# Performance work log

Hardware: AMD Instinct MI355X
Metric: run time of the kernel (lower is better)

## Reference

```python
import jax, jax.numpy as jnp
import numpy as np

EMB = 1024
HEADS = 16
HEAD_DIM = EMB // HEADS
SEQ = 2048
BATCH = 2
EPS = 1e-5


def gelu_tanh(x):
    # 0.5*x*(1+tanh(sqrt(2/pi)*(x+0.044715*x^3)))
    c = jnp.sqrt(jnp.asarray(2.0 / jnp.pi, x.dtype))
    return 0.5 * x * (1.0 + jnp.tanh(c * (x + 0.044715 * x * x * x)))


def layernorm(x, scale, shift):
    mean = jnp.mean(x, axis=-1, keepdims=True)
    # torch var(unbiased=True) -> ddof=1
    var = jnp.var(x, axis=-1, keepdims=True, ddof=1)
    return scale * (x - mean) / jnp.sqrt(var + EPS) + shift


def setup_inputs() -> dict:
    key = jax.random.key(0)
    ks = jax.random.split(key, 12)
    s = 0.02
    d = {
        "x": jax.random.normal(ks[0], (BATCH, SEQ, EMB), jnp.float32),
        "Wq": jax.random.normal(ks[1], (EMB, EMB), jnp.float32) * s,
        "bq": jnp.zeros((EMB,), jnp.float32),
        "Wk": jax.random.normal(ks[2], (EMB, EMB), jnp.float32) * s,
        "bk": jnp.zeros((EMB,), jnp.float32),
        "Wv": jax.random.normal(ks[3], (EMB, EMB), jnp.float32) * s,
        "bv": jnp.zeros((EMB,), jnp.float32),
        "Wo": jax.random.normal(ks[4], (EMB, EMB), jnp.float32) * s,
        "bo": jnp.zeros((EMB,), jnp.float32),
        "W1": jax.random.normal(ks[5], (EMB, 4 * EMB), jnp.float32) * s,
        "b1": jnp.zeros((4 * EMB,), jnp.float32),
        "W2": jax.random.normal(ks[6], (4 * EMB, EMB), jnp.float32) * s,
        "b2": jnp.zeros((EMB,), jnp.float32),
        "ln1_scale": jnp.ones((EMB,), jnp.float32),
        "ln1_shift": jnp.zeros((EMB,), jnp.float32),
        "ln2_scale": jnp.ones((EMB,), jnp.float32),
        "ln2_shift": jnp.zeros((EMB,), jnp.float32),
    }
    return d


def reference(x, Wq, bq, Wk, bk, Wv, bv, Wo, bo, W1, b1, W2, b2,
              ln1_scale, ln1_shift, ln2_scale, ln2_shift):
    b, n, _ = x.shape

    # --- attention sub-block (pre-norm) ---
    h = layernorm(x, ln1_scale, ln1_shift)
    q = (h @ Wq + bq).reshape(b, n, HEADS, HEAD_DIM).transpose(0, 2, 1, 3)
    k = (h @ Wk + bk).reshape(b, n, HEADS, HEAD_DIM).transpose(0, 2, 1, 3)
    v = (h @ Wv + bv).reshape(b, n, HEADS, HEAD_DIM).transpose(0, 2, 1, 3)

    # explicit O(n^2) scores, as in the source
    scores = jnp.einsum("bhqd,bhkd->bhqk", q, k)
    causal = jnp.triu(jnp.ones((n, n), bool), k=1)  # True above diagonal -> masked
    scores = jnp.where(causal, -jnp.inf, scores)
    weights = jax.nn.softmax(scores / jnp.sqrt(jnp.asarray(HEAD_DIM, x.dtype)), axis=-1)
    ctx = jnp.einsum("bhqk,bhkd->bhqd", weights, v)
    ctx = ctx.transpose(0, 2, 1, 3).reshape(b, n, EMB)
    x = x + (ctx @ Wo + bo)  # dropout is identity (rate 0 / eval)

    # --- FFN sub-block (pre-norm) ---
    h = layernorm(x, ln2_scale, ln2_shift)
    h = gelu_tanh(h @ W1 + b1)
    x = x + (h @ W2 + b2)
    return x
```

## Files before the change

kernel.cpp:

```cpp
#include <hip/hip_runtime.h>
#include <hip/hip_bf16.h>

#define EMB 1024
#define SEQ 2048
#define BATCH 2
#define HEADS 16
#define HDIM 64
#define ROWS (BATCH*SEQ)

typedef __hip_bfloat16 bf16;
typedef __bf16 bf16x8 __attribute__((ext_vector_type(8)));
typedef float f32x4 __attribute__((ext_vector_type(4)));

#define AS1 __attribute__((address_space(1)))
#define AS3 __attribute__((address_space(3)))

__device__ __forceinline__ void load_lds16(const void* g, void* l) {
    __builtin_amdgcn_global_load_lds((const AS1 void*)g, (AS3 void*)l, 16, 0, 0);
}

__device__ __forceinline__ float gelu_f(float x) {
    float y = 1.5957691216057308f * (x + 0.044715f * x * x * x);
    return x / (1.0f + __expf(-y));
}

__global__ void transpose_cast_kernel(const float* __restrict__ in, bf16* __restrict__ out,
                                      int R, int C) {
    __shared__ bf16 tile[32][33];
    int tx = threadIdx.x, ty = threadIdx.y;
    int c0 = blockIdx.x * 32, r0 = blockIdx.y * 32;
    for (int i = ty; i < 32; i += 8)
        tile[i][tx] = (bf16)in[(size_t)(r0 + i) * C + c0 + tx];
    __syncthreads();
    for (int i = ty; i < 32; i += 8)
        out[(size_t)(c0 + i) * R + r0 + tx] = tile[tx][i];
}

__global__ void transpose_cast4_kernel(const float* __restrict__ w0, const float* __restrict__ w1,
                                       const float* __restrict__ w2, const float* __restrict__ w3,
                                       bf16* __restrict__ o0, bf16* __restrict__ o1,
                                       bf16* __restrict__ o2, bf16* __restrict__ o3) {
    __shared__ bf16 tile[32][33];
    int z = blockIdx.z;
    const float* in = (z == 0) ? w0 : (z == 1) ? w1 : (z == 2) ? w2 : w3;
    bf16* out = (z == 0) ? o0 : (z == 1) ? o1 : (z == 2) ? o2 : o3;
    int tx = threadIdx.x, ty = threadIdx.y;
    int c0 = blockIdx.x * 32, r0 = blockIdx.y * 32;
    for (int i = ty; i < 32; i += 8)
        tile[i][tx] = (bf16)in[(size_t)(r0 + i) * 1024 + c0 + tx];
    __syncthreads();
    for (int i = ty; i < 32; i += 8)
        out[(size_t)(c0 + i) * 1024 + r0 + tx] = tile[tx][i];
}

__global__ void transpose_v_kernel(const bf16* __restrict__ v, bf16* __restrict__ vt) {
    __shared__ bf16 tile[32][33];
    int tx = threadIdx.x, ty = threadIdx.y;
    int bh = blockIdx.z;
    const bf16* in = v + (size_t)(bh >> 4) * SEQ * EMB + (bh & 15) * HDIM;
    bf16* out = vt + (size_t)bh * HDIM * SEQ;
    int s0 = blockIdx.x * 32, d0 = blockIdx.y * 32;
    for (int i = ty; i < 32; i += 8)
        tile[i][tx] = in[(size_t)(s0 + i) * EMB + d0 + tx];
    __syncthreads();
    for (int i = ty; i < 32; i += 8)
        out[(size_t)(d0 + i) * SEQ + s0 + tx] = tile[tx][i];
}

__global__ __launch_bounds__(256) void layernorm_kernel(const float* __restrict__ x,
                                                        bf16* __restrict__ out,
                                                        const float* __restrict__ scale,
                                                        const float* __restrict__ shift) {
    int row = blockIdx.x;
    int t = threadIdx.x;
    const float* xr = x + (size_t)row * EMB;
    float v[4];
    float s = 0.f, s2 = 0.f;
#pragma unroll
    for (int i = 0; i < 4; i++) {
        v[i] = xr[t + 256 * i];
        s += v[i];
        s2 += v[i] * v[i];
    }
#pragma unroll
    for (int off = 32; off > 0; off >>= 1) {
        s += __shfl_down(s, off);
        s2 += __shfl_down(s2, off);
    }
    __shared__ float sh[8];
    __shared__ float stats[2];
    int lane = t & 63, wid = t >> 6;
    if (lane == 0) { sh[wid] = s; sh[wid + 4] = s2; }
    __syncthreads();
    if (t == 0) {
        float ts = sh[0] + sh[1] + sh[2] + sh[3];
        float ts2 = sh[4] + sh[5] + sh[6] + sh[7];
        float mean = ts / (float)EMB;
        float var = (ts2 - (float)EMB * mean * mean) / (float)(EMB - 1);
        stats[0] = mean;
        stats[1] = rsqrtf(var + 1e-5f);
    }
    __syncthreads();
    float mean = stats[0], inv = stats[1];
#pragma unroll
    for (int i = 0; i < 4; i++) {
        int c = t + 256 * i;
        float y = (v[i] - mean) * inv * scale[c] + shift[c];
        out[(size_t)row * EMB + c] = (bf16)y;
    }
}

__device__ __forceinline__ void swz64(int id, int& bx, int& by) {
    int xcd = id & 7, m = id >> 3;
    by = xcd + 8 * (m & 3) + 32 * (m >> 6);
    bx = (m >> 2) & 15;
}

__device__ __forceinline__ void stage_half(const bf16* g, bf16* lds, int tid, size_t rowK64) {
    load_lds16(g, lds + tid * 8);
    load_lds16(g + rowK64, lds + 4096 + tid * 8);
}

template <int ACT, int QKV>
__global__ __launch_bounds__(512, 2) void gemm256_kernel(
    const bf16* __restrict__ A, const bf16* __restrict__ BT,
    bf16* __restrict__ C0, bf16* __restrict__ C1, bf16* __restrict__ C2,
    const float* __restrict__ bias0, const float* __restrict__ bias1,
    const float* __restrict__ bias2, int N, int K) {
    __shared__ __align__(16) bf16 lA[4][128 * 64];
    __shared__ __align__(16) bf16 lB[4][128 * 64];
    const int tid = threadIdx.x;
    const int wave = tid >> 6, lane = tid & 63;
    const int an = lane & 15, aq = lane >> 4;
    const int wr = wave >> 2, wc = wave & 3;

    int id = blockIdx.x;
    int xcd = id & 7, m = id >> 3;
    int by = xcd * 2 + (m & 1);
    int bx = m >> 1;
    int m0 = by * 256, n0 = bx * 256;

    const int srow = tid >> 3;
    const int csw = ((tid & 7) ^ (srow & 7)) * 8;
    const bf16* Ag = A + (size_t)(m0 + srow) * K + csw;
    const bf16* Bg = BT + (size_t)(n0 + srow) * K + csw;
    const size_t rowK64 = (size_t)64 * K;
    const size_t rowK128 = (size_t)128 * K;

    stage_half(Bg, lB[0], tid, rowK64);
    stage_half(Bg + rowK128, lB[1], tid, rowK64);
    stage_half(Ag, lA[0], tid, rowK64);
    stage_half(Ag + rowK128, lA[1], tid, rowK64);
    stage_half(Bg + 64, lB[2], tid, rowK64);
    stage_half(Bg + rowK128 + 64, lB[3], tid, rowK64);
    asm volatile("s_waitcnt vmcnt(4)" ::: "memory");
    __builtin_amdgcn_s_barrier();

    f32x4 acc[8][4] = {};
    const int NT = K >> 6;
    const int lrB = (wc & 1) * 64;

    for (int t = 0; t < NT; ++t) {
        const bf16* As = lA[(2 * t + wr) & 3];
        const bf16* Bs = lB[(2 * t + (wc >> 1)) & 3];
        bf16x8 bfv[4][2];
#pragma unroll
        for (int p = 0; p < 4; ++p) {
            bf16x8 af[2][2];
            if (p == 0) {
#pragma unroll
                for (int j = 0; j < 4; ++j)
#pragma unroll
                    for (int kk = 0; kk < 2; ++kk) {
                        int r = lrB + 16 * j + an;
                        bfv[j][kk] = *(const bf16x8*)(Bs + r * 64 + ((kk * 4 + aq) ^ (r & 7)) * 8);
                    }
            }
#pragma unroll
            for (int ii = 0; ii < 2; ++ii)
#pragma unroll
                for (int kk = 0; kk < 2; ++kk) {
                    int r = 16 * (2 * p + ii) + an;
                    af[ii][kk] = *(const bf16x8*)(As + r * 64 + ((kk * 4 + aq) ^ (r & 7)) * 8);
                }
            if (p == 0) {
                if (t + 1 < NT)
                    stage_half(Ag + (size_t)(t + 1) * 64, lA[(2 * t + 2) & 3], tid, rowK64);
            } else if (p == 1) {
                if (t + 1 < NT)
                    stage_half(Ag + rowK128 + (size_t)(t + 1) * 64, lA[(2 * t + 3) & 3], tid, rowK64);
            } else if (p == 2) {
                if (t + 2 < NT)
                    stage_half(Bg + (size_t)(t + 2) * 64, lB[(2 * t + 4) & 3], tid, rowK64);
            } else {
                if (t + 2 < NT) {
                    stage_half(Bg + rowK128 + (size_t)(t + 2) * 64, lB[(2 * t + 5) & 3], tid, rowK64);
                    asm volatile("s_waitcnt vmcnt(4)" ::: "memory");
                } else {
                    asm volatile("s_waitcnt vmcnt(0)" ::: "memory");
                }
            }
            __builtin_amdgcn_s_barrier();
            asm volatile("s_waitcnt lgkmcnt(0)" ::: "memory");
            __builtin_amdgcn_s_setprio(1);
#pragma unroll
            for (int ii = 0; ii < 2; ++ii)
#pragma unroll
                for (int j = 0; j < 4; ++j)
#pragma unroll
                    for (int kk = 0; kk < 2; ++kk)
                        acc[2 * p + ii][j] = __builtin_amdgcn_mfma_f32_16x16x32_bf16(
                            af[ii][kk], bfv[j][kk], acc[2 * p + ii][j], 0, 0, 0);
            __builtin_amdgcn_s_setprio(0);
            __builtin_amdgcn_s_barrier();
        }
    }

#pragma unroll
    for (int j = 0; j < 4; ++j) {
        int col = n0 + wc * 64 + 16 * j + an;
        if (QKV == 0) {
            float bv = bias0[col];
#pragma unroll
            for (int i = 0; i < 8; ++i) {
#pragma unroll
                for (int r = 0; r < 4; ++r) {
                    int row = m0 + wr * 128 + 16 * i + aq * 4 + r;
                    float v = acc[i][j][r] + bv;
                    if (ACT == 1) v = gelu_f(v);
                    C0[(size_t)row * N + col] = (bf16)v;
                }
            }
        } else {
            int region = col >> 10, c = col & 1023;
            const float* bp = (region == 0) ? bias0 : (region == 1) ? bias1 : bias2;
            bf16* outp = (region == 0) ? C0 : (region == 1) ? C1 : C2;
            float scl = (region == 0) ? 0.125f : 1.0f;
            float bv = bp[c];
#pragma unroll
            for (int i = 0; i < 8; ++i) {
#pragma unroll
                for (int r = 0; r < 4; ++r) {
                    int row = m0 + wr * 128 + 16 * i + aq * 4 + r;
                    float v = (acc[i][j][r] + bv) * scl;
                    outp[(size_t)row * EMB + c] = (bf16)v;
                }
            }
        }
    }
}

template <int RES, int OUTF>
__global__ __launch_bounds__(256) void gemm64_kernel(const bf16* __restrict__ A,
                                                     const bf16* __restrict__ BT,
                                                     void* __restrict__ Cout,
                                                     const float* __restrict__ bias,
                                                     const float* __restrict__ res,
                                                     int M, int N, int K) {
    __shared__ __align__(16) bf16 lA[2][2][64 * 32];
    __shared__ __align__(16) bf16 lB[2][2][64 * 32];
    int tid = threadIdx.x;
    int wave = tid >> 6, lane = tid & 63;
    int bx, by;
    swz64(blockIdx.x, bx, by);
    int m0 = by * 64, n0 = bx * 64;
    int wm = (wave >> 1) * 32, wn = (wave & 1) * 32;
    f32x4 acc[2][2] = {};

    int srow = wave * 16 + (lane >> 2);
    int skc = (lane & 3) * 8;
    const bf16* Ag = A + (size_t)(m0 + srow) * K + skc;
    const bf16* Bg = BT + (size_t)(n0 + srow) * K + skc;
    size_t woff = (size_t)(wave * 16) * 32;

    const int an = lane & 15;
    const int ak = (lane >> 4) * 8;

    load_lds16(Ag, &lA[0][0][woff]);
    load_lds16(Ag + 32, &lA[0][1][woff]);
    load_lds16(Bg, &lB[0][0][woff]);
    load_lds16(Bg + 32, &lB[0][1][woff]);

    int nsteps = K >> 6;
    for (int t = 0; t < nsteps; t++) {
        int buf = t & 1;
        asm volatile("s_waitcnt vmcnt(0)" ::: "memory");
        __syncthreads();
        if (t + 1 < nsteps) {
            int k0 = (t + 1) * 64;
            load_lds16(Ag + k0, &lA[buf ^ 1][0][woff]);
            load_lds16(Ag + k0 + 32, &lA[buf ^ 1][1][woff]);
            load_lds16(Bg + k0, &lB[buf ^ 1][0][woff]);
            load_lds16(Bg + k0 + 32, &lB[buf ^ 1][1][woff]);
        }
#pragma unroll
        for (int h = 0; h < 2; h++) {
            bf16x8 af[2], bfv[2];
#pragma unroll
            for (int i = 0; i < 2; i++)
                af[i] = *(const bf16x8*)(&lA[buf][h][(wm + 16 * i + an) * 32 + ak]);
#pragma unroll
            for (int j = 0; j < 2; j++)
                bfv[j] = *(const bf16x8*)(&lB[buf][h][(wn + 16 * j + an) * 32 + ak]);
#pragma unroll
            for (int i = 0; i < 2; i++)
#pragma unroll
                for (int j = 0; j < 2; j++)
                    acc[i][j] = __builtin_amdgcn_mfma_f32_16x16x32_bf16(af[i], bfv[j], acc[i][j], 0, 0, 0);
        }
    }
#pragma unroll
    for (int j = 0; j < 2; j++) {
        int col = n0 + wn + 16 * j + an;
        float bv = bias[col];
#pragma unroll
        for (int i = 0; i < 2; i++) {
#pragma unroll
            for (int r = 0; r < 4; r++) {
                int row = m0 + wm + 16 * i + (lane >> 4) * 4 + r;
                float vx = acc[i][j][r] + bv;
                size_t idx = (size_t)row * N + col;
                if (RES == 2) vx += res[idx];
                if (OUTF == 0) ((bf16*)Cout)[idx] = (bf16)vx;
                else ((float*)Cout)[idx] = vx;
            }
        }
    }
}

__global__ __launch_bounds__(256) void attn_kernel(const bf16* __restrict__ q,
                                                   const bf16* __restrict__ k,
                                                   const bf16* __restrict__ vt,
                                                   bf16* __restrict__ ctx) {
    __shared__ __align__(16) bf16 ksm[2][2048];
    __shared__ __align__(16) bf16 vsm[2][2048];
    __shared__ __align__(16) bf16 pbuf[4][16][32];
    int tid = threadIdx.x;
    int wave = tid >> 6, lane = tid & 63;
    int id = blockIdx.x;
    int bh = id >> 5;
    int bx = ((id & 31) + bh) & 31;
    int b = bh >> 4, h = bh & 15;
    int q0 = bx * 64 + wave * 16;
    const bf16* qp = q + (size_t)b * SEQ * EMB + h * HDIM;
    const bf16* kp = k + (size_t)b * SEQ * EMB + h * HDIM;
    const bf16* vp = vt + (size_t)bh * HDIM * SEQ;

    int an = lane & 15;
    int aq = lane >> 4;
    bf16x8 qf0 = *(const bf16x8*)(qp + (size_t)(q0 + an) * EMB + aq * 8);
    bf16x8 qf1 = *(const bf16x8*)(qp + (size_t)(q0 + an) * EMB + 32 + aq * 8);
    f32x4 o[4] = {};
    float lp[4] = {0.f, 0.f, 0.f, 0.f};

    const bf16* kg = kp + (size_t)((wave & 1) * 16 + (lane >> 2)) * EMB + ((wave & 2) ? 32 : 0) + (lane & 3) * 8;
    const bf16* vg = vp + (size_t)(wave * 16 + (lane >> 2)) * SEQ + (lane & 3) * 8;

    int nsteps = 2 * bx + 2;
    load_lds16(kg, (char*)ksm[0] + wave * 1024);
    load_lds16(vg, (char*)vsm[0] + wave * 1024);

    for (int t = 0; t < nsteps; t++) {
        int buf = t & 1;
        asm volatile("s_waitcnt vmcnt(0)" ::: "memory");
        __syncthreads();
        if (t + 1 < nsteps) {
            int kvn = (t + 1) * 32;
            load_lds16(kg + (size_t)kvn * EMB, (char*)ksm[buf ^ 1] + wave * 1024);
            load_lds16(vg + kvn, (char*)vsm[buf ^ 1] + wave * 1024);
        }
        const char* kb = (const char*)ksm[buf];
        bf16x8 kf0 = *(const bf16x8*)(kb + an * 64 + aq * 16);
        bf16x8 kf1 = *(const bf16x8*)(kb + 2048 + an * 64 + aq * 16);
        bf16x8 kf2 = *(const bf16x8*)(kb + (16 + an) * 64 + aq * 16);
        bf16x8 kf3 = *(const bf16x8*)(kb + 2048 + (16 + an) * 64 + aq * 16);
        f32x4 s0 = {}, s1 = {};
        s0 = __builtin_amdgcn_mfma_f32_16x16x32_bf16(qf0, kf0, s0, 0, 0, 0);
        s0 = __builtin_amdgcn_mfma_f32_16x16x32_bf16(qf1, kf1, s0, 0, 0, 0);
        s1 = __builtin_amdgcn_mfma_f32_16x16x32_bf16(qf0, kf2, s1, 0, 0, 0);
        s1 = __builtin_amdgcn_mfma_f32_16x16x32_bf16(qf1, kf3, s1, 0, 0, 0);
        int kv = t * 32;
        if (t < nsteps - 2) {
#pragma unroll
            for (int r = 0; r < 4; r++) {
                float p0 = __expf(s0[r]);
                float p1 = __expf(s1[r]);
                lp[r] += p0 + p1;
                pbuf[wave][aq * 4 + r][an] = (bf16)p0;
                pbuf[wave][aq * 4 + r][16 + an] = (bf16)p1;
            }
        } else {
#pragma unroll
            for (int r = 0; r < 4; r++) {
                int row = q0 + aq * 4 + r;
                float p0 = (kv + an > row) ? 0.f : __expf(s0[r]);
                float p1 = (kv + 16 + an > row) ? 0.f : __expf(s1[r]);
                lp[r] += p0 + p1;
                pbuf[wave][aq * 4 + r][an] = (bf16)p0;
                pbuf[wave][aq * 4 + r][16 + an] = (bf16)p1;
            }
        }
        asm volatile("s_waitcnt lgkmcnt(0)" ::: "memory");
        bf16x8 pa = *(const bf16x8*)(&pbuf[wave][an][aq * 8]);
        const char* vb = (const char*)vsm[buf];
#pragma unroll
        for (int dt = 0; dt < 4; dt++) {
            bf16x8 vf = *(const bf16x8*)(vb + (dt * 16 + an) * 64 + aq * 16);
            o[dt] = __builtin_amdgcn_mfma_f32_16x16x32_bf16(pa, vf, o[dt], 0, 0, 0);
        }
    }
#pragma unroll
    for (int r = 0; r < 4; r++) {
        float v = lp[r];
        v += __shfl_xor(v, 1);
        v += __shfl_xor(v, 2);
        v += __shfl_xor(v, 4);
        v += __shfl_xor(v, 8);
        lp[r] = v;
    }
#pragma unroll
    for (int dt = 0; dt < 4; dt++) {
#pragma unroll
        for (int r = 0; r < 4; r++) {
            int row = q0 + aq * 4 + r;
            int col = h * HDIM + dt * 16 + an;
            ctx[((size_t)b * SEQ + row) * EMB + col] = (bf16)(o[dt][r] / lp[r]);
        }
    }
}

extern "C" void kernel_launch(void* const* d_in, const int* in_sizes, int n_in,
                              void* d_out, int out_size, void* d_ws, size_t ws_size,
                              hipStream_t stream) {
    const float* x = (const float*)d_in[0];
    const float* Wq = (const float*)d_in[1];
    const float* bq = (const float*)d_in[2];
    const float* Wk = (const float*)d_in[3];
    const float* bk = (const float*)d_in[4];
    const float* Wv = (const float*)d_in[5];
    const float* bv = (const float*)d_in[6];
    const float* Wo = (const float*)d_in[7];
    const float* bo = (const float*)d_in[8];
    const float* W1 = (const float*)d_in[9];
    const float* b1 = (const float*)d_in[10];
    const float* W2 = (const float*)d_in[11];
    const float* b2 = (const float*)d_in[12];
    const float* ln1s = (const float*)d_in[13];
    const float* ln1b = (const float*)d_in[14];
    const float* ln2s = (const float*)d_in[15];
    const float* ln2b = (const float*)d_in[16];
    float* out = (float*)d_out;

    char* ws = (char*)d_ws;
    const size_t MB = 1ull << 20;
    bf16* WqT = (bf16*)(ws + 0 * MB);
    bf16* WkT = (bf16*)(ws + 2 * MB);
    bf16* WvT = (bf16*)(ws + 4 * MB);
    bf16* WoT = (bf16*)(ws + 6 * MB);
    bf16* W1T = (bf16*)(ws + 8 * MB);
    bf16* W2T = (bf16*)(ws + 16 * MB);
    bf16* hbuf = (bf16*)(ws + 24 * MB);
    bf16* qbuf = (bf16*)(ws + 32 * MB);
    bf16* kbuf = (bf16*)(ws + 40 * MB);
    bf16* vbuf = (bf16*)(ws + 48 * MB);
    bf16* vtb = (bf16*)(ws + 56 * MB);
    bf16* ctxb = (bf16*)(ws + 64 * MB);
    float* x1 = (float*)(ws + 72 * MB);
    bf16* hff = (bf16*)(ws + 32 * MB);

    dim3 tb(32, 8);
    transpose_cast4_kernel<<<dim3(32, 32, 4), tb, 0, stream>>>(Wq, Wk, Wv, Wo, WqT, WkT, WvT, WoT);
    transpose_cast_kernel<<<dim3(128, 32), tb, 0, stream>>>(W1, W1T, 1024, 4096);
    transpose_cast_kernel<<<dim3(32, 128), tb, 0, stream>>>(W2, W2T, 4096, 1024);

    layernorm_kernel<<<ROWS, 256, 0, stream>>>(x, hbuf, ln1s, ln1b);

    gemm256_kernel<0, 1><<<192, 512, 0, stream>>>(hbuf, WqT, qbuf, kbuf, vbuf,
                                                  bq, bk, bv, EMB, EMB);

    transpose_v_kernel<<<dim3(64, 2, 32), tb, 0, stream>>>(vbuf, vtb);

    attn_kernel<<<1024, 256, 0, stream>>>(qbuf, kbuf, vtb, ctxb);

    gemm64_kernel<2, 1><<<1024, 256, 0, stream>>>(ctxb, WoT, x1, bo, x, ROWS, EMB, EMB);

    layernorm_kernel<<<ROWS, 256, 0, stream>>>(x1, hbuf, ln2s, ln2b);

    gemm256_kernel<1, 0><<<256, 512, 0, stream>>>(hbuf, W1T, hff, nullptr, nullptr,
                                                  b1, nullptr, nullptr, 4 * EMB, EMB);

    gemm64_kernel<2, 1><<<1024, 256, 0, stream>>>(hff, W2T, out, b2, x1, ROWS, EMB, 4 * EMB);
}
```

Baseline: 367.4 us.

## Enlarge attention KV tile to 64 with XOR-swizzled LDS layout

The attention kernel now stages 64 keys and values per step instead of 32, which halves the number of barrier-separated iterations. K and V tiles in LDS use an XOR swizzle on 16-byte chunks to avoid bank conflicts, and the P buffer row is padded to 40 elements. The causal mask is applied only on the final step, and launch bounds request 4 blocks per CU. In exchange, LDS use per block doubles, which may limit occupancy. The diagonal step now does more wasted masked work.

```diff
diff --git a/kernel.cpp b/kernel.cpp
--- a/kernel.cpp
+++ b/kernel.cpp
@@ -328,13 +328,13 @@
     }
 }
 
-__global__ __launch_bounds__(256) void attn_kernel(const bf16* __restrict__ q,
-                                                   const bf16* __restrict__ k,
-                                                   const bf16* __restrict__ vt,
-                                                   bf16* __restrict__ ctx) {
-    __shared__ __align__(16) bf16 ksm[2][2048];
-    __shared__ __align__(16) bf16 vsm[2][2048];
-    __shared__ __align__(16) bf16 pbuf[4][16][32];
+__global__ __launch_bounds__(256, 4) void attn_kernel(const bf16* __restrict__ q,
+                                                      const bf16* __restrict__ k,
+                                                      const bf16* __restrict__ vt,
+                                                      bf16* __restrict__ ctx) {
+    __shared__ __align__(16) bf16 ksm[2][64 * 64];
+    __shared__ __align__(16) bf16 vsm[2][64 * 64];
+    __shared__ __align__(16) bf16 pbuf[4][16][40];
     int tid = threadIdx.x;
     int wave = tid >> 6, lane = tid & 63;
     int id = blockIdx.x;
@@ -346,69 +346,81 @@
     const bf16* kp = k + (size_t)b * SEQ * EMB + h * HDIM;
     const bf16* vp = vt + (size_t)bh * HDIM * SEQ;
 
-    int an = lane & 15;
-    int aq = lane >> 4;
+    int an = lane & 15, aq = lane >> 4;
+
     bf16x8 qf0 = *(const bf16x8*)(qp + (size_t)(q0 + an) * EMB + aq * 8);
     bf16x8 qf1 = *(const bf16x8*)(qp + (size_t)(q0 + an) * EMB + 32 + aq * 8);
     f32x4 o[4] = {};
     float lp[4] = {0.f, 0.f, 0.f, 0.f};
 
-    const bf16* kg = kp + (size_t)((wave & 1) * 16 + (lane >> 2)) * EMB + ((wave & 2) ? 32 : 0) + (lane & 3) * 8;
-    const bf16* vg = vp + (size_t)(wave * 16 + (lane >> 2)) * SEQ + (lane & 3) * 8;
-
-    int nsteps = 2 * bx + 2;
-    load_lds16(kg, (char*)ksm[0] + wave * 1024);
-    load_lds16(vg, (char*)vsm[0] + wave * 1024);
-
-    for (int t = 0; t < nsteps; t++) {
+    int srow0 = tid >> 3;
+    int srow1 = srow0 + 32;
+    int sc = tid & 7;
+    const bf16* kg0 = kp + (size_t)srow0 * EMB + ((sc ^ (srow0 & 7)) * 8);
+    const bf16* kg1 = kp + (size_t)srow1 * EMB + ((sc ^ (srow1 & 7)) * 8);
+    const bf16* vg0 = vp + (size_t)srow0 * SEQ + ((sc ^ (srow0 & 7)) * 8);
+    const bf16* vg1 = vp + (size_t)srow1 * SEQ + ((sc ^ (srow1 & 7)) * 8);
+
+    int nsteps = bx + 1;
+
+    load_lds16(kg0, ksm[0] + tid * 8);
+    load_lds16(kg1, ksm[0] + (256 + tid) * 8);
+    load_lds16(vg0, vsm[0] + tid * 8);
+    load_lds16(vg1, vsm[0] + (256 + tid) * 8);
+    asm volatile("s_waitcnt vmcnt(0)" ::: "memory");
+    __syncthreads();
+
+    auto step = [&](int t, bool last_) {
         int buf = t & 1;
-        asm volatile("s_waitcnt vmcnt(0)" ::: "memory");
-        __syncthreads();
-        if (t + 1 < nsteps) {
-            int kvn = (t + 1) * 32;
-            load_lds16(kg + (size_t)kvn * EMB, (char*)ksm[buf ^ 1] + wave * 1024);
-            load_lds16(vg + kvn, (char*)vsm[buf ^ 1] + wave * 1024);
-        }
-        const char* kb = (const char*)ksm[buf];
-        bf16x8 kf0 = *(const bf16x8*)(kb + an * 64 + aq * 16);
-        bf16x8 kf1 = *(const bf16x8*)(kb + 2048 + an * 64 + aq * 16);
-        bf16x8 kf2 = *(const bf16x8*)(kb + (16 + an) * 64 + aq * 16);
-        bf16x8 kf3 = *(const bf16x8*)(kb + 2048 + (16 + an) * 64 + aq * 16);
-        f32x4 s0 = {}, s1 = {};
-        s0 = __builtin_amdgcn_mfma_f32_16x16x32_bf16(qf0, kf0, s0, 0, 0, 0);
-        s0 = __builtin_amdgcn_mfma_f32_16x16x32_bf16(qf1, kf1, s0, 0, 0, 0);
-        s1 = __builtin_amdgcn_mfma_f32_16x16x32_bf16(qf0, kf2, s1, 0, 0, 0);
-        s1 = __builtin_amdgcn_mfma_f32_16x16x32_bf16(qf1, kf3, s1, 0, 0, 0);
-        int kv = t * 32;
-        if (t < nsteps - 2) {
-#pragma unroll
-            for (int r = 0; r < 4; r++) {
-                float p0 = __expf(s0[r]);
-                float p1 = __expf(s1[r]);
-                lp[r] += p0 + p1;
-                pbuf[wave][aq * 4 + r][an] = (bf16)p0;
-                pbuf[wave][aq * 4 + r][16 + an] = (bf16)p1;
-            }
-        } else {
-#pragma unroll
-            for (int r = 0; r < 4; r++) {
-                int row = q0 + aq * 4 + r;
-                float p0 = (kv + an > row) ? 0.f : __expf(s0[r]);
-                float p1 = (kv + 16 + an > row) ? 0.f : __expf(s1[r]);
-                lp[r] += p0 + p1;
-                pbuf[wave][aq * 4 + r][an] = (bf16)p0;
-                pbuf[wave][aq * 4 + r][16 + an] = (bf16)p1;
-            }
-        }
-        asm volatile("s_waitcnt lgkmcnt(0)" ::: "memory");
-        bf16x8 pa = *(const bf16x8*)(&pbuf[wave][an][aq * 8]);
-        const char* vb = (const char*)vsm[buf];
-#pragma unroll
-        for (int dt = 0; dt < 4; dt++) {
-            bf16x8 vf = *(const bf16x8*)(vb + (dt * 16 + an) * 64 + aq * 16);
-            o[dt] = __builtin_amdgcn_mfma_f32_16x16x32_bf16(pa, vf, o[dt], 0, 0, 0);
-        }
-    }
+        if (!last_) {
+            size_t ko = (size_t)(t + 1) * 64 * EMB;
+            int vo = (t + 1) * 64;
+            load_lds16(kg0 + ko, ksm[buf ^ 1] + tid * 8);
+            load_lds16(kg1 + ko, ksm[buf ^ 1] + (256 + tid) * 8);
+            load_lds16(vg0 + vo, vsm[buf ^ 1] + tid * 8);
+            load_lds16(vg1 + vo, vsm[buf ^ 1] + (256 + tid) * 8);
+        }
+        const bf16* kb = ksm[buf];
+        const bf16* vb = vsm[buf];
+        int kvbase = t * 64;
+#pragma unroll
+        for (int hh = 0; hh < 2; hh++) {
+#pragma unroll
+            for (int nbl = 0; nbl < 2; nbl++) {
+                int nb = hh * 2 + nbl;
+                int krow = nb * 16 + an;
+                bf16x8 kfa = *(const bf16x8*)(kb + krow * 64 + ((aq ^ (an & 7)) * 8));
+                bf16x8 kfb = *(const bf16x8*)(kb + krow * 64 + (((4 + aq) ^ (an & 7)) * 8));
+                f32x4 s = {};
+                s = __builtin_amdgcn_mfma_f32_16x16x32_bf16(qf0, kfa, s, 0, 0, 0);
+                s = __builtin_amdgcn_mfma_f32_16x16x32_bf16(qf1, kfb, s, 0, 0, 0);
+                int kvg = kvbase + nb * 16 + an;
+#pragma unroll
+                for (int r = 0; r < 4; r++) {
+                    float p = __expf(s[r]);
+                    if (last_ && (kvg > q0 + aq * 4 + r)) p = 0.f;
+                    lp[r] += p;
+                    pbuf[wave][aq * 4 + r][nbl * 16 + an] = (bf16)p;
+                }
+            }
+            asm volatile("s_waitcnt lgkmcnt(0)" ::: "memory");
+            bf16x8 pa = *(const bf16x8*)(&pbuf[wave][an][aq * 8]);
+#pragma unroll
+            for (int dt = 0; dt < 4; dt++) {
+                int drow = dt * 16 + an;
+                bf16x8 vf = *(const bf16x8*)(vb + drow * 64 + (((hh * 4 + aq) ^ (an & 7)) * 8));
+                o[dt] = __builtin_amdgcn_mfma_f32_16x16x32_bf16(pa, vf, o[dt], 0, 0, 0);
+            }
+        }
+        if (!last_) {
+            asm volatile("s_waitcnt vmcnt(0)" ::: "memory");
+            __syncthreads();
+        }
+    };
+
+    for (int t = 0; t < nsteps - 1; t++) step(t, false);
+    step(nsteps - 1, true);
+
 #pragma unroll
     for (int r = 0; r < 4; r++) {
         float v = lp[r];
```

Measured after the change: 354.4 us. 3.5% less time.
